# Optimization experiments

Hardware: AMD Instinct MI355X
Metric: run time of the kernel (lower is better)

The kernel has to match this reference:

```python
import jax, jax.numpy as jnp
import numpy as np

N_NODES = 100000
N_EDGES = 1600000
N_GRAPHS = 64
D_IN = 128
D_HID = 128
PERM = 128
N_CLS = 8


def _sage_conv(h, src, dst, W_self, W_neigh, b, n_nodes):
    # DGL SAGEConv 'mean': fc_self(h) + fc_neigh(mean of in-neighbor feats) + bias
    agg = jax.ops.segment_sum(h[src], dst, num_segments=n_nodes)          # [N, d]
    deg = jax.ops.segment_sum(jnp.ones((src.shape[0],), h.dtype), dst,
                              num_segments=n_nodes)                        # [N]
    mean = agg / jnp.maximum(deg, 1.0)[:, None]                            # zero-deg nodes -> 0
    return h @ W_self + mean @ W_neigh + b


def setup_inputs() -> dict:
    key = jax.random.key(0)
    ks = jax.random.split(key, 12)
    s = 1.0 / np.sqrt(D_IN)
    inp = {
        'h': jax.random.normal(ks[0], (N_NODES, D_IN), jnp.float32),
        'perm_features': jax.random.normal(ks[1], (N_GRAPHS, PERM), jnp.float32),
        'src': jax.random.randint(ks[2], (N_EDGES,), 0, N_NODES),
        'dst': jax.random.randint(ks[3], (N_EDGES,), 0, N_NODES),
        'graph_ids': jnp.sort(jax.random.randint(ks[4], (N_NODES,), 0, N_GRAPHS)),
        'W1_self': jax.random.normal(ks[5], (D_IN, D_HID), jnp.float32) * s,
        'W1_neigh': jax.random.normal(ks[6], (D_IN, D_HID), jnp.float32) * s,
        'b1': jnp.zeros((D_HID,), jnp.float32),
        'W2_self': jax.random.normal(ks[7], (D_HID, D_HID), jnp.float32) * s,
        'W2_neigh': jax.random.normal(ks[8], (D_HID, D_HID), jnp.float32) * s,
        'b2': jnp.zeros((D_HID,), jnp.float32),
        'Wc': jax.random.normal(ks[9], (D_HID + PERM, N_CLS), jnp.float32) * s,
        'bc': jnp.zeros((N_CLS,), jnp.float32),
    }
    return inp


def reference(h, perm_features, src, dst, graph_ids,
              W1_self, W1_neigh, b1, W2_self, W2_neigh, b2, Wc, bc):
    n = h.shape[0]
    h1 = jax.nn.relu(_sage_conv(h, src, dst, W1_self, W1_neigh, b1, n))
    h2 = _sage_conv(h1, src, dst, W2_self, W2_neigh, b2, n)
    # dgl.mean_nodes: per-graph mean of node features
    gsum = jax.ops.segment_sum(h2, graph_ids, num_segments=N_GRAPHS)       # [B, d]
    gcnt = jax.ops.segment_sum(jnp.ones((n,), h.dtype), graph_ids,
                               num_segments=N_GRAPHS)                       # [B]
    hg = gsum / jnp.maximum(gcnt, 1.0)[:, None]
    combined = jnp.concatenate([hg, perm_features], axis=1)                 # [B, d+perm]
    return combined @ Wc + bc
```

## Files before the change

### kernel.cpp

```cpp
#include <hip/hip_runtime.h>

#define DID 128
#define NCLS 8
#define NPB 512
#define NPB_SHIFT 9
#define NBLK 512
#define CAP 12288
#define PCHUNK 64

typedef __attribute__((ext_vector_type(8))) short bf16x8;
typedef __attribute__((ext_vector_type(4))) float f32x4;
typedef __attribute__((ext_vector_type(8))) unsigned short u16x8;

static __device__ __forceinline__ unsigned short f2bf(float f) {
  union { float f; unsigned int u; } x;
  x.f = f;
  unsigned int r = (x.u + 0x7fffu + ((x.u >> 16) & 1u)) >> 16;
  return (unsigned short)r;
}
static __device__ __forceinline__ float bfhi(unsigned int v) {
  union { unsigned int u; float f; } x;
  x.u = v & 0xffff0000u;
  return x.f;
}
static __device__ __forceinline__ float bflo(unsigned int v) {
  union { unsigned int u; float f; } x;
  x.u = v << 16;
  return x.f;
}

__global__ __launch_bounds__(256) void kB_hist(const int* __restrict__ dst,
                                               int* __restrict__ hist, int E,
                                               int nbuk) {
  __shared__ int c[256];
  int tid = threadIdx.x;
  for (int i = tid; i < nbuk; i += 256) c[i] = 0;
  __syncthreads();
  int epb = (E + NBLK - 1) / NBLK;
  int e0 = blockIdx.x * epb;
  int e1 = min(E, e0 + epb);
  for (int e = e0 + tid; e < e1; e += 256)
    atomicAdd(&c[dst[e] >> NPB_SHIFT], 1);
  __syncthreads();
  for (int i = tid; i < nbuk; i += 256)
    hist[(size_t)i * NBLK + blockIdx.x] = c[i];
}

__global__ void k_scan1(const int* __restrict__ deg, int* __restrict__ rp,
                        int* __restrict__ part, int n) {
  __shared__ int sd[256];
  int t = threadIdx.x;
  int base = blockIdx.x * 1024 + t * 4;
  int v0 = (base + 0 < n) ? deg[base + 0] : 0;
  int v1 = (base + 1 < n) ? deg[base + 1] : 0;
  int v2 = (base + 2 < n) ? deg[base + 2] : 0;
  int v3 = (base + 3 < n) ? deg[base + 3] : 0;
  int ts = v0 + v1 + v2 + v3;
  sd[t] = ts;
  __syncthreads();
  for (int off = 1; off < 256; off <<= 1) {
    int x = 0;
    if (t >= off) x = sd[t - off];
    __syncthreads();
    if (t >= off) sd[t] += x;
    __syncthreads();
  }
  int excl = sd[t] - ts;
  if (base + 0 < n) rp[base + 0] = excl;
  if (base + 1 < n) rp[base + 1] = excl + v0;
  if (base + 2 < n) rp[base + 2] = excl + v0 + v1;
  if (base + 3 < n) rp[base + 3] = excl + v0 + v1 + v2;
  if (t == 255) part[blockIdx.x] = sd[255];
}

__global__ void k_scan2(int* __restrict__ part, int nblk) {
  __shared__ int sd[1024];
  int t = threadIdx.x;
  int v = (t < nblk) ? part[t] : 0;
  sd[t] = v;
  __syncthreads();
  for (int off = 1; off < 1024; off <<= 1) {
    int x = 0;
    if (t >= off) x = sd[t - off];
    __syncthreads();
    if (t >= off) sd[t] += x;
    __syncthreads();
  }
  if (t < nblk) part[t] = sd[t] - v;
}

__global__ void k_scan3(int* __restrict__ rp, const int* __restrict__ part,
                        int n, int E) {
  int t = threadIdx.x;
  int add = part[blockIdx.x];
  int base = blockIdx.x * 1024 + t * 4;
#pragma unroll
  for (int i = 0; i < 4; ++i)
    if (base + i < n) rp[base + i] += add;
  if (blockIdx.x == 0 && t == 0) rp[n] = E;
}

__global__ __launch_bounds__(256) void kB_scat(const int* __restrict__ src,
                                               const int* __restrict__ dst,
                                               const int* __restrict__ off,
                                               unsigned long long* __restrict__ pairs,
                                               int E, int nbuk) {
  __shared__ int cur[256];
  int tid = threadIdx.x;
  for (int i = tid; i < nbuk; i += 256)
    cur[i] = off[(size_t)i * NBLK + blockIdx.x];
  __syncthreads();
  int epb = (E + NBLK - 1) / NBLK;
  int e0 = blockIdx.x * epb;
  int e1 = min(E, e0 + epb);
  for (int e = e0 + tid; e < e1; e += 256) {
    int s = src[e];
    int d = dst[e];
    int p = atomicAdd(&cur[d >> NPB_SHIFT], 1);
    pairs[p] = ((unsigned long long)(unsigned)d << 32) | (unsigned)s;
  }
}

__global__ __launch_bounds__(512) void kB_build(
    const unsigned long long* __restrict__ pairs, const int* __restrict__ off,
    int* __restrict__ rp, int* __restrict__ col, int N, int nbuk, int E) {
  __shared__ int cnt[NPB];
  __shared__ int exc[NPB];
  __shared__ int colstage[CAP];
  int tid = threadIdx.x;
  int b = blockIdx.x;
  int eb = off[(size_t)b * NBLK];
  int ee = off[(size_t)(b + 1) * NBLK];
  int m = ee - eb;

  cnt[tid] = 0;
  __syncthreads();
  for (int i = eb + tid; i < ee; i += NPB) {
    int d = (int)(pairs[i] >> 32);
    atomicAdd(&cnt[d & (NPB - 1)], 1);
  }
  __syncthreads();
  exc[tid] = cnt[tid];
  __syncthreads();
  for (int o = 1; o < NPB; o <<= 1) {
    int v = (tid >= o) ? exc[tid - o] : 0;
    __syncthreads();
    exc[tid] += v;
    __syncthreads();
  }
  int myexc = exc[tid] - cnt[tid];
  int node = b * NPB + tid;
  if (node < N) rp[node] = eb + myexc;
  if (b == nbuk - 1 && tid == 0) rp[N] = E;
  __syncthreads();
  cnt[tid] = myexc;
  __syncthreads();
  if (m <= CAP) {
    for (int i = eb + tid; i < ee; i += NPB) {
      unsigned long long pr = pairs[i];
      int d = (int)(pr >> 32);
      int s = (int)(pr & 0xffffffffu);
      int p = atomicAdd(&cnt[d & (NPB - 1)], 1);
      colstage[p] = s;
    }
    __syncthreads();
    for (int i = tid; i < m; i += NPB) col[eb + i] = colstage[i];
  } else {
    for (int i = eb + tid; i < ee; i += NPB) {
      unsigned long long pr = pairs[i];
      int d = (int)(pr >> 32);
      int s = (int)(pr & 0xffffffffu);
      int p = atomicAdd(&cnt[d & (NPB - 1)], 1);
      col[eb + p] = s;
    }
  }
}

__global__ void k_h2b(const float* __restrict__ h, unsigned short* __restrict__ hb,
                      int total8) {
  int i = blockIdx.x * 256 + threadIdx.x;
  if (i >= total8) return;
  const float4* h4 = (const float4*)h;
  float4 a = h4[(size_t)i * 2];
  float4 b = h4[(size_t)i * 2 + 1];
  u16x8 o;
  o[0] = f2bf(a.x); o[1] = f2bf(a.y); o[2] = f2bf(a.z); o[3] = f2bf(a.w);
  o[4] = f2bf(b.x); o[5] = f2bf(b.y); o[6] = f2bf(b.z); o[7] = f2bf(b.w);
  *(u16x8*)(hb + (size_t)i * 8) = o;
}

__global__ void k_pack4(const float* __restrict__ W0, const float* __restrict__ W1,
                        const float* __restrict__ W2, const float* __restrict__ W3,
                        unsigned short* __restrict__ P0, unsigned short* __restrict__ P1,
                        unsigned short* __restrict__ P2, unsigned short* __restrict__ P3) {
  int gid = blockIdx.x * 256 + threadIdx.x;
  int m = gid >> 14;
  int idx = gid & 16383;
  int j = idx & 7;
  int l = (idx >> 3) & 63;
  int kf = (idx >> 9) & 3;
  int ct = idx >> 11;
  int colc = ct * 16 + (l & 15);
  int k = kf * 32 + (l >> 4) * 8 + j;
  const float* W = (m == 0) ? W0 : (m == 1) ? W1 : (m == 2) ? W2 : W3;
  unsigned short* P = (m == 0) ? P0 : (m == 1) ? P1 : (m == 2) ? P2 : P3;
  P[idx] = f2bf(W[k * 128 + colc]);
}

__global__ __launch_bounds__(256, 2) void k_gemm2(
    const unsigned short* __restrict__ hb, const unsigned short* __restrict__ WpS,
    const unsigned short* __restrict__ WpN, float* __restrict__ z,
    unsigned short* __restrict__ yb, int n) {
  const int l = threadIdx.x & 63;
  const int w = threadIdx.x >> 6;
  const int rowW = blockIdx.x * 128 + w * 32;
  const int cl = l & 15;
  const int cg = l >> 4;

  bf16x8 A[2][4];
#pragma unroll
  for (int rt = 0; rt < 2; ++rt) {
    int row = rowW + rt * 16 + cl;
#pragma unroll
    for (int kf = 0; kf < 4; ++kf) {
      if (row < n)
        A[rt][kf] = *(const bf16x8*)(hb + (size_t)row * 128 + kf * 32 + cg * 8);
      else
        A[rt][kf] = (bf16x8){0, 0, 0, 0, 0, 0, 0, 0};
    }
  }

  f32x4 accS[2][8], accN[2][8];
#pragma unroll
  for (int rt = 0; rt < 2; ++rt)
#pragma unroll
    for (int ct = 0; ct < 8; ++ct) {
      accS[rt][ct] = (f32x4){0.f, 0.f, 0.f, 0.f};
      accN[rt][ct] = (f32x4){0.f, 0.f, 0.f, 0.f};
    }

#pragma unroll
  for (int ct = 0; ct < 8; ++ct) {
    bf16x8 BS[4], BN[4];
#pragma unroll
    for (int kf = 0; kf < 4; ++kf) {
      BS[kf] = *(const bf16x8*)(WpS + ((ct * 4 + kf) * 64 + l) * 8);
      BN[kf] = *(const bf16x8*)(WpN + ((ct * 4 + kf) * 64 + l) * 8);
    }
#pragma unroll
    for (int rt = 0; rt < 2; ++rt)
#pragma unroll
      for (int kf = 0; kf < 4; ++kf) {
        accS[rt][ct] =
            __builtin_amdgcn_mfma_f32_16x16x32_bf16(A[rt][kf], BS[kf], accS[rt][ct], 0, 0, 0);
        accN[rt][ct] =
            __builtin_amdgcn_mfma_f32_16x16x32_bf16(A[rt][kf], BN[kf], accN[rt][ct], 0, 0, 0);
      }
  }

#pragma unroll
  for (int rt = 0; rt < 2; ++rt)
#pragma unroll
    for (int ct = 0; ct < 8; ++ct) {
#pragma unroll
      for (int r = 0; r < 4; ++r) {
        int row = rowW + rt * 16 + cg * 4 + r;
        if (row < n) {
          int colc = ct * 16 + cl;
          z[(size_t)row * 128 + colc] = accS[rt][ct][r];
          yb[(size_t)row * 128 + colc] = f2bf(accN[rt][ct][r]);
        }
      }
    }
}

template <int OUTMODE>
__global__ __launch_bounds__(256, 8) void k_aggr2(
    const unsigned int* __restrict__ Y, const float* Z,
    const int* __restrict__ rp, const int* __restrict__ col,
    const float* __restrict__ bias, void* outp, int n) {
  int wid = (blockIdx.x * 256 + threadIdx.x) >> 6;
  int lane = threadIdx.x & 63;
  if (wid >= n) return;
  int s = rp[wid], e = rp[wid + 1];
  float ax = 0.f, ay = 0.f;
  int i = s;
  for (; i + 8 <= e; i += 8) {
    unsigned int v0 = Y[(size_t)col[i + 0] * 64 + lane];
    unsigned int v1 = Y[(size_t)col[i + 1] * 64 + lane];
    unsigned int v2 = Y[(size_t)col[i + 2] * 64 + lane];
    unsigned int v3 = Y[(size_t)col[i + 3] * 64 + lane];
    unsigned int v4 = Y[(size_t)col[i + 4] * 64 + lane];
    unsigned int v5 = Y[(size_t)col[i + 5] * 64 + lane];
    unsigned int v6 = Y[(size_t)col[i + 6] * 64 + lane];
    unsigned int v7 = Y[(size_t)col[i + 7] * 64 + lane];
    ax += bflo(v0) + bflo(v1) + bflo(v2) + bflo(v3) + bflo(v4) + bflo(v5) +
          bflo(v6) + bflo(v7);
    ay += bfhi(v0) + bfhi(v1) + bfhi(v2) + bfhi(v3) + bfhi(v4) + bfhi(v5) +
          bfhi(v6) + bfhi(v7);
  }
  for (; i + 4 <= e; i += 4) {
    unsigned int v0 = Y[(size_t)col[i + 0] * 64 + lane];
    unsigned int v1 = Y[(size_t)col[i + 1] * 64 + lane];
    unsigned int v2 = Y[(size_t)col[i + 2] * 64 + lane];
    unsigned int v3 = Y[(size_t)col[i + 3] * 64 + lane];
    ax += bflo(v0) + bflo(v1) + bflo(v2) + bflo(v3);
    ay += bfhi(v0) + bfhi(v1) + bfhi(v2) + bfhi(v3);
  }
  for (; i < e; ++i) {
    unsigned int v = Y[(size_t)col[i] * 64 + lane];
    ax += bflo(v);
    ay += bfhi(v);
  }
  int deg = e - s;
  float scale = 1.0f / (float)(deg > 1 ? deg : 1);
  float2 zv = ((const float2*)Z)[(size_t)wid * 64 + lane];
  float2 bb = ((const float2*)bias)[lane];
  float ox = zv.x + ax * scale + bb.x;
  float oy = zv.y + ay * scale + bb.y;
  if (OUTMODE == 1) {
    ox = fmaxf(ox, 0.f);
    oy = fmaxf(oy, 0.f);
    unsigned int packed = (unsigned int)f2bf(ox) | ((unsigned int)f2bf(oy) << 16);
    ((unsigned int*)outp)[(size_t)wid * 64 + lane] = packed;
  } else {
    ((float2*)outp)[(size_t)wid * 64 + lane] = make_float2(ox, oy);
  }
}

__global__ void k_bounds(const int* __restrict__ gids, int* __restrict__ gs,
                         int n, int NG) {
  int g = threadIdx.x;
  if (g < NG) {
    int lo = 0, hi = n;
    while (lo < hi) {
      int m = (lo + hi) >> 1;
      if (gids[m] < g) lo = m + 1;
      else hi = m;
    }
    gs[g] = lo;
  } else if (g == NG) {
    gs[NG] = n;
  }
}

__global__ __launch_bounds__(256) void k_pool(const float* __restrict__ H2,
                                              const int* __restrict__ gs,
                                              float* __restrict__ gsum, int NG) {
  int g = blockIdx.x / PCHUNK;
  int c = blockIdx.x % PCHUNK;
  int t = threadIdx.x;
  int s = gs[g], e = gs[g + 1];
  int cnt = e - s;
  int per = (cnt + PCHUNK - 1) / PCHUNK;
  int rs = s + c * per;
  int re = rs + per < e ? rs + per : e;
  if (rs >= re) return;
  int rslot = t >> 5;
  int d4 = t & 31;
  const float4* H4 = (const float4*)H2;
  float4 acc = make_float4(0.f, 0.f, 0.f, 0.f);
  for (int r = rs + rslot; r < re; r += 8) {
    float4 v = H4[(size_t)r * 32 + d4];
    acc.x += v.x; acc.y += v.y; acc.z += v.z; acc.w += v.w;
  }
  __shared__ float4 sacc[256];
  sacc[t] = acc;
  __syncthreads();
#pragma unroll
  for (int o = 4; o >= 1; o >>= 1) {
    if (rslot < o) {
      float4 a = sacc[t];
      float4 b = sacc[t + o * 32];
      a.x += b.x; a.y += b.y; a.z += b.z; a.w += b.w;
      sacc[t] = a;
    }
    __syncthreads();
  }
  if (t < 32) {
    float4 a = sacc[t];
    atomicAdd(&gsum[g * DID + t * 4 + 0], a.x);
    atomicAdd(&gsum[g * DID + t * 4 + 1], a.y);
    atomicAdd(&gsum[g * DID + t * 4 + 2], a.z);
    atomicAdd(&gsum[g * DID + t * 4 + 3], a.w);
  }
}

__global__ void k_head(const float* __restrict__ gsum,
                       const float* __restrict__ perm,
                       const float* __restrict__ Wc,
                       const float* __restrict__ bc,
                       const int* __restrict__ gs, float* __restrict__ out,
                       int NG) {
  int t = threadIdx.x;
  if (t >= NG * NCLS) return;
  int g = t >> 3, c = t & 7;
  int cnt = gs[g + 1] - gs[g];
  float inv = 1.0f / (float)(cnt > 1 ? cnt : 1);
  float acc = bc[c];
#pragma unroll 4
  for (int k = 0; k < DID; ++k)
    acc += gsum[g * DID + k] * inv * Wc[k * NCLS + c];
#pragma unroll 4
  for (int k = 0; k < DID; ++k)
    acc += perm[g * DID + k] * Wc[(DID + k) * NCLS + c];
  out[g * NCLS + c] = acc;
}

extern "C" void kernel_launch(void* const* d_in, const int* in_sizes, int n_in,
                              void* d_out, int out_size, void* d_ws,
                              size_t ws_size, hipStream_t stream) {
  const float* h = (const float*)d_in[0];
  const float* perm = (const float*)d_in[1];
  const int* src = (const int*)d_in[2];
  const int* dst = (const int*)d_in[3];
  const int* gids = (const int*)d_in[4];
  const float* W1s = (const float*)d_in[5];
  const float* W1n = (const float*)d_in[6];
  const float* b1 = (const float*)d_in[7];
  const float* W2s = (const float*)d_in[8];
  const float* W2n = (const float*)d_in[9];
  const float* b2 = (const float*)d_in[10];
  const float* Wc = (const float*)d_in[11];
  const float* bc = (const float*)d_in[12];
  float* out = (float*)d_out;

  const int N = in_sizes[0] / DID;
  const int E = in_sizes[2];
  const int NG = in_sizes[1] / DID;
  const int nbuk = (N + NPB - 1) >> NPB_SHIFT;
  const int nscan = nbuk * NBLK;

  char* w = (char*)d_ws;
  size_t off_ = 0;
  auto alloc = [&](size_t bytes) -> void* {
    off_ = (off_ + 511) & ~(size_t)511;
    void* p = w + off_;
    off_ += bytes;
    return p;
  };
  float* gsum = (float*)alloc((size_t)NG * DID * 4);
  size_t zbytes = off_;
  int* hist = (int*)alloc((size_t)nscan * 4);
  int* boff = (int*)alloc((size_t)(nscan + 1) * 4);
  int* part = (int*)alloc(1024 * 4);
  int* rp = (int*)alloc((size_t)(N + 1) * 4);
  int* gs = (int*)alloc((size_t)(NG + 1) * 4);
  int* col = (int*)alloc((size_t)E * 4);
  unsigned long long* pairs = (unsigned long long*)alloc((size_t)E * 8);
  unsigned short* hb = (unsigned short*)alloc((size_t)N * DID * 2);
  unsigned short* yb = (unsigned short*)alloc((size_t)N * DID * 2);
  float* z = (float*)alloc((size_t)N * DID * 4);
  unsigned short* Wp1s = (unsigned short*)alloc(128 * 128 * 2);
  unsigned short* Wp1n = (unsigned short*)alloc(128 * 128 * 2);
  unsigned short* Wp2s = (unsigned short*)alloc(128 * 128 * 2);
  unsigned short* Wp2n = (unsigned short*)alloc(128 * 128 * 2);

  hipMemsetAsync(d_ws, 0, zbytes, stream);

  const int nchunk = (nscan + 1023) / 1024;
  const int ngb = (N + 127) / 128;
  const int nagg = (N + 3) / 4;
  const int ncvt = ((N * DID / 8) + 255) / 256;

  k_h2b<<<ncvt, 256, 0, stream>>>(h, hb, N * DID / 8);
  k_pack4<<<256, 256, 0, stream>>>(W1s, W1n, W2s, W2n, Wp1s, Wp1n, Wp2s, Wp2n);

  kB_hist<<<NBLK, 256, 0, stream>>>(dst, hist, E, nbuk);
  k_scan1<<<nchunk, 256, 0, stream>>>(hist, boff, part, nscan);
  k_scan2<<<1, 1024, 0, stream>>>(part, nchunk);
  k_scan3<<<nchunk, 256, 0, stream>>>(boff, part, nscan, E);
  kB_scat<<<NBLK, 256, 0, stream>>>(src, dst, boff, pairs, E, nbuk);
  kB_build<<<nbuk, NPB, 0, stream>>>(pairs, boff, rp, col, N, nbuk, E);

  k_gemm2<<<ngb, 256, 0, stream>>>(hb, Wp1s, Wp1n, z, yb, N);
  k_aggr2<1><<<nagg, 256, 0, stream>>>((const unsigned int*)yb, z, rp, col, b1,
                                       (void*)hb, N);

  k_gemm2<<<ngb, 256, 0, stream>>>(hb, Wp2s, Wp2n, z, yb, N);
  k_aggr2<0><<<nagg, 256, 0, stream>>>((const unsigned int*)yb, z, rp, col, b2,
                                       (void*)z, N);

  k_bounds<<<1, 128, 0, stream>>>(gids, gs, N, NG);
  k_pool<<<NG * PCHUNK, 256, 0, stream>>>(z, gs, gsum, NG);
  k_head<<<1, 512, 0, stream>>>(gsum, perm, Wc, bc, gs, out, NG);
}
```

Measured before the change: 415.2 us.

## Fuse prep kernels, pack edge pairs to 32 bits, split GEMM columns

Merges the bf16 conversion, weight packing, destination histogram and gsum zeroing into one multi-role launch, replacing a memset and three kernel launches. Edge pairs are packed into 32 bits (local dst in the high bits, src in the low 23) instead of 64, halving scatter and build traffic. This only holds while node ids fit in 23 bits. The GEMM grid now splits columns in two per row block, with fewer accumulators and a higher occupancy bound. The graph-bounds kernel is dropped in favour of binary searches inside pool and head, and NBLK is halved.

```diff
diff --git a/kernel.cpp b/kernel.cpp
--- a/kernel.cpp
+++ b/kernel.cpp
@@ -4,7 +4,7 @@
 #define NCLS 8
 #define NPB 512
 #define NPB_SHIFT 9
-#define NBLK 512
+#define NBLK 256
 #define CAP 12288
 #define PCHUNK 64
 
@@ -28,22 +28,66 @@
   x.u = v << 16;
   return x.f;
 }
-
-__global__ __launch_bounds__(256) void kB_hist(const int* __restrict__ dst,
-                                               int* __restrict__ hist, int E,
-                                               int nbuk) {
+static __device__ __forceinline__ int lowerb(const int* __restrict__ a, int n,
+                                             int key) {
+  int lo = 0, hi = n;
+  while (lo < hi) {
+    int m = (lo + hi) >> 1;
+    if (a[m] < key) lo = m + 1;
+    else hi = m;
+  }
+  return lo;
+}
+
+__global__ __launch_bounds__(256) void k_prep(
+    const float* __restrict__ h, unsigned short* __restrict__ hb, int total8,
+    int ncvt, const float* __restrict__ W0, const float* __restrict__ W1,
+    const float* __restrict__ W2, const float* __restrict__ W3,
+    unsigned short* __restrict__ P0, unsigned short* __restrict__ P1,
+    unsigned short* __restrict__ P2, unsigned short* __restrict__ P3,
+    const int* __restrict__ dst, int* __restrict__ hist, int E, int nbuk,
+    float* __restrict__ gsum, int ngsum) {
   __shared__ int c[256];
+  int bid = blockIdx.x;
   int tid = threadIdx.x;
-  for (int i = tid; i < nbuk; i += 256) c[i] = 0;
-  __syncthreads();
-  int epb = (E + NBLK - 1) / NBLK;
-  int e0 = blockIdx.x * epb;
-  int e1 = min(E, e0 + epb);
-  for (int e = e0 + tid; e < e1; e += 256)
-    atomicAdd(&c[dst[e] >> NPB_SHIFT], 1);
-  __syncthreads();
-  for (int i = tid; i < nbuk; i += 256)
-    hist[(size_t)i * NBLK + blockIdx.x] = c[i];
+  if (bid < ncvt) {
+    int i = bid * 256 + tid;
+    if (i >= total8) return;
+    const float4* h4 = (const float4*)h;
+    float4 a = h4[(size_t)i * 2];
+    float4 b = h4[(size_t)i * 2 + 1];
+    u16x8 o;
+    o[0] = f2bf(a.x); o[1] = f2bf(a.y); o[2] = f2bf(a.z); o[3] = f2bf(a.w);
+    o[4] = f2bf(b.x); o[5] = f2bf(b.y); o[6] = f2bf(b.z); o[7] = f2bf(b.w);
+    *(u16x8*)(hb + (size_t)i * 8) = o;
+  } else if (bid < ncvt + 256) {
+    int gid = (bid - ncvt) * 256 + tid;
+    int m = gid >> 14;
+    int idx = gid & 16383;
+    int j = idx & 7;
+    int l = (idx >> 3) & 63;
+    int kf = (idx >> 9) & 3;
+    int ct = idx >> 11;
+    int colc = ct * 16 + (l & 15);
+    int k = kf * 32 + (l >> 4) * 8 + j;
+    const float* W = (m == 0) ? W0 : (m == 1) ? W1 : (m == 2) ? W2 : W3;
+    unsigned short* P = (m == 0) ? P0 : (m == 1) ? P1 : (m == 2) ? P2 : P3;
+    P[idx] = f2bf(W[k * 128 + colc]);
+  } else if (bid < ncvt + 256 + NBLK) {
+    int b = bid - ncvt - 256;
+    for (int i = tid; i < nbuk; i += 256) c[i] = 0;
+    __syncthreads();
+    int epb = (E + NBLK - 1) / NBLK;
+    int e0 = b * epb;
+    int e1 = min(E, e0 + epb);
+    for (int e = e0 + tid; e < e1; e += 256)
+      atomicAdd(&c[dst[e] >> NPB_SHIFT], 1);
+    __syncthreads();
+    for (int i = tid; i < nbuk; i += 256)
+      hist[(size_t)i * NBLK + b] = c[i];
+  } else {
+    for (int i = tid; i < ngsum; i += 256) gsum[i] = 0.f;
+  }
 }
 
 __global__ void k_scan1(const int* __restrict__ deg, int* __restrict__ rp,
@@ -103,7 +147,7 @@
 __global__ __launch_bounds__(256) void kB_scat(const int* __restrict__ src,
                                                const int* __restrict__ dst,
                                                const int* __restrict__ off,
-                                               unsigned long long* __restrict__ pairs,
+                                               unsigned int* __restrict__ pairs,
                                                int E, int nbuk) {
   __shared__ int cur[256];
   int tid = threadIdx.x;
@@ -117,12 +161,12 @@
     int s = src[e];
     int d = dst[e];
     int p = atomicAdd(&cur[d >> NPB_SHIFT], 1);
-    pairs[p] = ((unsigned long long)(unsigned)d << 32) | (unsigned)s;
+    pairs[p] = ((unsigned)(d & (NPB - 1)) << 23) | (unsigned)s;
   }
 }
 
 __global__ __launch_bounds__(512) void kB_build(
-    const unsigned long long* __restrict__ pairs, const int* __restrict__ off,
+    const unsigned int* __restrict__ pairs, const int* __restrict__ off,
     int* __restrict__ rp, int* __restrict__ col, int N, int nbuk, int E) {
   __shared__ int cnt[NPB];
   __shared__ int exc[NPB];
@@ -136,8 +180,8 @@
   cnt[tid] = 0;
   __syncthreads();
   for (int i = eb + tid; i < ee; i += NPB) {
-    int d = (int)(pairs[i] >> 32);
-    atomicAdd(&cnt[d & (NPB - 1)], 1);
+    int dl = (int)(pairs[i] >> 23);
+    atomicAdd(&cnt[dl], 1);
   }
   __syncthreads();
   exc[tid] = cnt[tid];
@@ -157,63 +201,34 @@
   __syncthreads();
   if (m <= CAP) {
     for (int i = eb + tid; i < ee; i += NPB) {
-      unsigned long long pr = pairs[i];
-      int d = (int)(pr >> 32);
-      int s = (int)(pr & 0xffffffffu);
-      int p = atomicAdd(&cnt[d & (NPB - 1)], 1);
+      unsigned int pr = pairs[i];
+      int dl = (int)(pr >> 23);
+      int s = (int)(pr & 0x7fffffu);
+      int p = atomicAdd(&cnt[dl], 1);
       colstage[p] = s;
     }
     __syncthreads();
     for (int i = tid; i < m; i += NPB) col[eb + i] = colstage[i];
   } else {
     for (int i = eb + tid; i < ee; i += NPB) {
-      unsigned long long pr = pairs[i];
-      int d = (int)(pr >> 32);
-      int s = (int)(pr & 0xffffffffu);
-      int p = atomicAdd(&cnt[d & (NPB - 1)], 1);
+      unsigned int pr = pairs[i];
+      int dl = (int)(pr >> 23);
+      int s = (int)(pr & 0x7fffffu);
+      int p = atomicAdd(&cnt[dl], 1);
       col[eb + p] = s;
     }
   }
 }
 
-__global__ void k_h2b(const float* __restrict__ h, unsigned short* __restrict__ hb,
-                      int total8) {
-  int i = blockIdx.x * 256 + threadIdx.x;
-  if (i >= total8) return;
-  const float4* h4 = (const float4*)h;
-  float4 a = h4[(size_t)i * 2];
-  float4 b = h4[(size_t)i * 2 + 1];
-  u16x8 o;
-  o[0] = f2bf(a.x); o[1] = f2bf(a.y); o[2] = f2bf(a.z); o[3] = f2bf(a.w);
-  o[4] = f2bf(b.x); o[5] = f2bf(b.y); o[6] = f2bf(b.z); o[7] = f2bf(b.w);
-  *(u16x8*)(hb + (size_t)i * 8) = o;
-}
-
-__global__ void k_pack4(const float* __restrict__ W0, const float* __restrict__ W1,
-                        const float* __restrict__ W2, const float* __restrict__ W3,
-                        unsigned short* __restrict__ P0, unsigned short* __restrict__ P1,
-                        unsigned short* __restrict__ P2, unsigned short* __restrict__ P3) {
-  int gid = blockIdx.x * 256 + threadIdx.x;
-  int m = gid >> 14;
-  int idx = gid & 16383;
-  int j = idx & 7;
-  int l = (idx >> 3) & 63;
-  int kf = (idx >> 9) & 3;
-  int ct = idx >> 11;
-  int colc = ct * 16 + (l & 15);
-  int k = kf * 32 + (l >> 4) * 8 + j;
-  const float* W = (m == 0) ? W0 : (m == 1) ? W1 : (m == 2) ? W2 : W3;
-  unsigned short* P = (m == 0) ? P0 : (m == 1) ? P1 : (m == 2) ? P2 : P3;
-  P[idx] = f2bf(W[k * 128 + colc]);
-}
-
-__global__ __launch_bounds__(256, 2) void k_gemm2(
+__global__ __launch_bounds__(256, 4) void k_gemm2(
     const unsigned short* __restrict__ hb, const unsigned short* __restrict__ WpS,
     const unsigned short* __restrict__ WpN, float* __restrict__ z,
     unsigned short* __restrict__ yb, int n) {
   const int l = threadIdx.x & 63;
   const int w = threadIdx.x >> 6;
-  const int rowW = blockIdx.x * 128 + w * 32;
+  const int rb = blockIdx.x >> 1;
+  const int cb = blockIdx.x & 1;
+  const int rowW = rb * 128 + w * 32;
   const int cl = l & 15;
   const int cg = l >> 4;
 
@@ -230,22 +245,23 @@
     }
   }
 
-  f32x4 accS[2][8], accN[2][8];
+  f32x4 accS[2][4], accN[2][4];
 #pragma unroll
   for (int rt = 0; rt < 2; ++rt)
 #pragma unroll
-    for (int ct = 0; ct < 8; ++ct) {
+    for (int ct = 0; ct < 4; ++ct) {
       accS[rt][ct] = (f32x4){0.f, 0.f, 0.f, 0.f};
       accN[rt][ct] = (f32x4){0.f, 0.f, 0.f, 0.f};
     }
 
 #pragma unroll
-  for (int ct = 0; ct < 8; ++ct) {
+  for (int ct = 0; ct < 4; ++ct) {
+    int ctg = cb * 4 + ct;
     bf16x8 BS[4], BN[4];
 #pragma unroll
     for (int kf = 0; kf < 4; ++kf) {
-      BS[kf] = *(const bf16x8*)(WpS + ((ct * 4 + kf) * 64 + l) * 8);
-      BN[kf] = *(const bf16x8*)(WpN + ((ct * 4 + kf) * 64 + l) * 8);
+      BS[kf] = *(const bf16x8*)(WpS + ((ctg * 4 + kf) * 64 + l) * 8);
+      BN[kf] = *(const bf16x8*)(WpN + ((ctg * 4 + kf) * 64 + l) * 8);
     }
 #pragma unroll
     for (int rt = 0; rt < 2; ++rt)
@@ -261,12 +277,12 @@
 #pragma unroll
   for (int rt = 0; rt < 2; ++rt)
 #pragma unroll
-    for (int ct = 0; ct < 8; ++ct) {
+    for (int ct = 0; ct < 4; ++ct) {
+      int colc = (cb * 4 + ct) * 16 + cl;
 #pragma unroll
       for (int r = 0; r < 4; ++r) {
         int row = rowW + rt * 16 + cg * 4 + r;
         if (row < n) {
-          int colc = ct * 16 + cl;
           z[(size_t)row * 128 + colc] = accS[rt][ct][r];
           yb[(size_t)row * 128 + colc] = f2bf(accN[rt][ct][r]);
         }
@@ -328,29 +344,14 @@
   }
 }
 
-__global__ void k_bounds(const int* __restrict__ gids, int* __restrict__ gs,
-                         int n, int NG) {
-  int g = threadIdx.x;
-  if (g < NG) {
-    int lo = 0, hi = n;
-    while (lo < hi) {
-      int m = (lo + hi) >> 1;
-      if (gids[m] < g) lo = m + 1;
-      else hi = m;
-    }
-    gs[g] = lo;
-  } else if (g == NG) {
-    gs[NG] = n;
-  }
-}
-
 __global__ __launch_bounds__(256) void k_pool(const float* __restrict__ H2,
-                                              const int* __restrict__ gs,
-                                              float* __restrict__ gsum, int NG) {
+                                              const int* __restrict__ gids,
+                                              float* __restrict__ gsum, int N) {
   int g = blockIdx.x / PCHUNK;
   int c = blockIdx.x % PCHUNK;
   int t = threadIdx.x;
-  int s = gs[g], e = gs[g + 1];
+  int s = lowerb(gids, N, g);
+  int e = lowerb(gids, N, g + 1);
   int cnt = e - s;
   int per = (cnt + PCHUNK - 1) / PCHUNK;
   int rs = s + c * per;
@@ -390,12 +391,12 @@
                        const float* __restrict__ perm,
                        const float* __restrict__ Wc,
                        const float* __restrict__ bc,
-                       const int* __restrict__ gs, float* __restrict__ out,
-                       int NG) {
+                       const int* __restrict__ gids, float* __restrict__ out,
+                       int N, int NG) {
   int t = threadIdx.x;
   if (t >= NG * NCLS) return;
   int g = t >> 3, c = t & 7;
-  int cnt = gs[g + 1] - gs[g];
+  int cnt = lowerb(gids, N, g + 1) - lowerb(gids, N, g);
   float inv = 1.0f / (float)(cnt > 1 ? cnt : 1);
   float acc = bc[c];
 #pragma unroll 4
@@ -440,14 +441,12 @@
     return p;
   };
   float* gsum = (float*)alloc((size_t)NG * DID * 4);
-  size_t zbytes = off_;
   int* hist = (int*)alloc((size_t)nscan * 4);
   int* boff = (int*)alloc((size_t)(nscan + 1) * 4);
   int* part = (int*)alloc(1024 * 4);
   int* rp = (int*)alloc((size_t)(N + 1) * 4);
-  int* gs = (int*)alloc((size_t)(NG + 1) * 4);
   int* col = (int*)alloc((size_t)E * 4);
-  unsigned long long* pairs = (unsigned long long*)alloc((size_t)E * 8);
+  unsigned int* pairs = (unsigned int*)alloc((size_t)E * 4);
   unsigned short* hb = (unsigned short*)alloc((size_t)N * DID * 2);
   unsigned short* yb = (unsigned short*)alloc((size_t)N * DID * 2);
   float* z = (float*)alloc((size_t)N * DID * 4);
@@ -456,32 +455,30 @@
   unsigned short* Wp2s = (unsigned short*)alloc(128 * 128 * 2);
   unsigned short* Wp2n = (unsigned short*)alloc(128 * 128 * 2);
 
-  hipMemsetAsync(d_ws, 0, zbytes, stream);
-
   const int nchunk = (nscan + 1023) / 1024;
-  const int ngb = (N + 127) / 128;
+  const int ngb2 = ((N + 127) / 128) * 2;
   const int nagg = (N + 3) / 4;
-  const int ncvt = ((N * DID / 8) + 255) / 256;
-
-  k_h2b<<<ncvt, 256, 0, stream>>>(h, hb, N * DID / 8);
-  k_pack4<<<256, 256, 0, stream>>>(W1s, W1n, W2s, W2n, Wp1s, Wp1n, Wp2s, Wp2n);
-
-  kB_hist<<<NBLK, 256, 0, stream>>>(dst, hist, E, nbuk);
+  const int total8 = N * DID / 8;
+  const int ncvt = (total8 + 255) / 256;
+
+  k_prep<<<ncvt + 256 + NBLK + 1, 256, 0, stream>>>(
+      h, hb, total8, ncvt, W1s, W1n, W2s, W2n, Wp1s, Wp1n, Wp2s, Wp2n, dst,
+      hist, E, nbuk, gsum, NG * DID);
+
   k_scan1<<<nchunk, 256, 0, stream>>>(hist, boff, part, nscan);
   k_scan2<<<1, 1024, 0, stream>>>(part, nchunk);
   k_scan3<<<nchunk, 256, 0, stream>>>(boff, part, nscan, E);
   kB_scat<<<NBLK, 256, 0, stream>>>(src, dst, boff, pairs, E, nbuk);
   kB_build<<<nbuk, NPB, 0, stream>>>(pairs, boff, rp, col, N, nbuk, E);
 
-  k_gemm2<<<ngb, 256, 0, stream>>>(hb, Wp1s, Wp1n, z, yb, N);
+  k_gemm2<<<ngb2, 256, 0, stream>>>(hb, Wp1s, Wp1n, z, yb, N);
   k_aggr2<1><<<nagg, 256, 0, stream>>>((const unsigned int*)yb, z, rp, col, b1,
                                        (void*)hb, N);
 
-  k_gemm2<<<ngb, 256, 0, stream>>>(hb, Wp2s, Wp2n, z, yb, N);
+  k_gemm2<<<ngb2, 256, 0, stream>>>(hb, Wp2s, Wp2n, z, yb, N);
   k_aggr2<0><<<nagg, 256, 0, stream>>>((const unsigned int*)yb, z, rp, col, b2,
                                        (void*)z, N);
 
-  k_bounds<<<1, 128, 0, stream>>>(gids, gs, N, NG);
-  k_pool<<<NG * PCHUNK, 256, 0, stream>>>(z, gs, gsum, NG);
-  k_head<<<1, 512, 0, stream>>>(gsum, perm, Wc, bc, gs, out, NG);
-}
+  k_pool<<<NG * PCHUNK, 256, 0, stream>>>(z, gids, gsum, N);
+  k_head<<<1, 512, 0, stream>>>(gsum, perm, Wc, bc, gids, out, N, NG);
+}
```

Result: no change. 421.0 us (+1.4%).
